# Kernel tuning notes

Measured on AMD Instinct MI355X. Metric: run time of the kernel, lower is better.

The kernel has to match this reference:

```python
import jax, jax.numpy as jnp
import numpy as np

N, E, IN, OUT = 50000, 800000, 128, 128
R = 5  # num_rels + 1 (last slice is the self-loop weight)


def setup_inputs() -> dict:
    key = jax.random.key(0)
    k = jax.random.split(key, 6)
    x = jax.random.normal(k[0], (N, IN), jnp.float32)
    src = jax.random.randint(k[1], (E,), 0, N)
    dst = jax.random.randint(k[2], (E,), 0, N)
    rel = jax.random.randint(k[3], (E,), 0, R - 1)  # edge rel_type in [0, num_rels)
    xavier = np.sqrt(2.0) * np.sqrt(6.0 / (IN + OUT))  # gain('relu') * xavier bound scale
    weight = jax.random.uniform(k[4], (R, IN, OUT), jnp.float32, -xavier, xavier)
    bias = jax.random.uniform(k[5], (R, OUT), jnp.float32, -xavier, xavier)
    return dict(x=x, weight=weight, bias=bias, src=src, dst=dst, rel=rel)


def reference(x, weight, bias, src, dst, rel):
    num_nodes = x.shape[0]
    num_edge_rels = weight.shape[0] - 1
    x_src = x[src]  # [E, IN] per-edge source gather
    # Per-edge message: x_src @ weight[rel] + bias[rel].
    # Grouped-GEMM style: one dense GEMM per relation, select by mask
    # (avoids materializing [E, IN, OUT] per-edge weights).
    msg = jnp.zeros((src.shape[0], weight.shape[2]), x.dtype)
    for r in range(num_edge_rels):
        hr = x_src @ weight[r] + bias[r]  # [E, OUT]
        msg = jnp.where((rel == r)[:, None], hr, msg)
    # Max-aggregation onto destination nodes; DGL fills 0 for nodes w/o in-edges.
    agg = jax.ops.segment_max(msg, dst, num_segments=num_nodes)  # [N, OUT]
    deg = jax.ops.segment_sum(jnp.ones_like(dst, jnp.float32), dst, num_segments=num_nodes)
    agg = jnp.where((deg > 0)[:, None], agg, jnp.zeros((), x.dtype))
    # Self-loop transform with last weight/bias slice.
    h = x @ weight[-1] + bias[-1] + agg
    return h
```

## Files before the change

### kernel.cpp

```cpp
#include <hip/hip_runtime.h>

#define NNODES 50000
#define NEDGES 800000
#define DIM    128
#define NRELS  4
#define NBLK2  25
#define DBLK   128
#define NDB    (5*DBLK)
#define NFB    3125
#define EPB    12500
#define NHC    64
#define RNG    25000

typedef __attribute__((ext_vector_type(8))) short bf16x8;
typedef __attribute__((ext_vector_type(8))) unsigned short u16x8;
typedef __attribute__((ext_vector_type(4))) float f32x4;

#define SSRC_OFF 0
#define CNT_OFF  3200000
#define BSUM_OFF 3404800
#define RANK_OFF 3405056
#define PCNT_OFF 5005056
#define WT_OFF   11405056
#define XBF_OFF  11568896
#define H_OFF    24368896

__device__ __forceinline__ unsigned short f2bf(float f) {
  unsigned u = __float_as_uint(f);
  return (unsigned short)((u + 0x7FFFu + ((u >> 16) & 1u)) >> 16);
}

__global__ void k_prep(const float* __restrict__ x, unsigned short* __restrict__ xbf,
                       const float* __restrict__ W, unsigned short* __restrict__ Wt) {
  int i = blockIdx.x * blockDim.x + threadIdx.x;
  if (i < NNODES * DIM / 8) {
    const float4* p = (const float4*)x + i * 2;
    float4 v0 = p[0], v1 = p[1];
    u16x8 o;
    o[0] = f2bf(v0.x); o[1] = f2bf(v0.y); o[2] = f2bf(v0.z); o[3] = f2bf(v0.w);
    o[4] = f2bf(v1.x); o[5] = f2bf(v1.y); o[6] = f2bf(v1.z); o[7] = f2bf(v1.w);
    *(u16x8*)(xbf + i * 8) = o;
  }
  if (i < 5 * DIM * DIM) {
    int r = i >> 14, rem = i & 16383, k = rem >> 7, c = rem & 127;
    Wt[(r << 14) + (c << 7) + k] = f2bf(W[i]);
  }
}

__global__ __launch_bounds__(1024) void k_hist(const int* __restrict__ dst,
                                               unsigned short* __restrict__ rank,
                                               unsigned short* __restrict__ pcnt) {
  __shared__ unsigned lh[RNG / 2];
  int c = blockIdx.x >> 1;
  int r0 = (blockIdx.x & 1) * RNG;
  for (int i = threadIdx.x; i < RNG / 2; i += 1024) lh[i] = 0u;
  __syncthreads();
  int e0 = c * EPB;
  for (int e = e0 + threadIdx.x; e < e0 + EPB; e += 1024) {
    int d = dst[e] - r0;
    if ((unsigned)d < (unsigned)RNG) {
      unsigned old = atomicAdd(&lh[d >> 1], (d & 1) ? 65536u : 1u);
      rank[e] = (unsigned short)((old >> ((d & 1) << 4)) & 0xFFFFu);
    }
  }
  __syncthreads();
  unsigned* prow = (unsigned*)(pcnt + (size_t)c * NNODES + r0);
  for (int i = threadIdx.x; i < RNG / 2; i += 1024) prow[i] = lh[i];
}

__global__ void k_scanB(unsigned short* __restrict__ pcnt, unsigned* __restrict__ cnt,
                        unsigned* __restrict__ bsum) {
  __shared__ unsigned sh[256];
  int tid = threadIdx.x;
  int bin0 = blockIdx.x * 2048 + tid * 8;
  unsigned run[8] = {0, 0, 0, 0, 0, 0, 0, 0};
  if (bin0 < NNODES) {
    for (int b = 0; b < NHC; b++) {
      size_t off = (size_t)b * NNODES + bin0;
      u16x8 v = *(const u16x8*)(pcnt + off);
      u16x8 w;
#pragma unroll
      for (int j = 0; j < 8; j++) { w[j] = (unsigned short)run[j]; run[j] += v[j]; }
      *(u16x8*)(pcnt + off) = w;
    }
  }
  unsigned tsum = 0;
#pragma unroll
  for (int j = 0; j < 8; j++) tsum += run[j];
  sh[tid] = tsum;
  __syncthreads();
  for (int off = 1; off < 256; off <<= 1) {
    unsigned t = (tid >= off) ? sh[tid - off] : 0u;
    __syncthreads();
    sh[tid] += t;
    __syncthreads();
  }
  unsigned r = sh[tid] - tsum;
#pragma unroll
  for (int j = 0; j < 8; j++) { unsigned t = run[j]; cnt[bin0 + j] = r; r += t; }
  if (tid == 255) bsum[blockIdx.x] = sh[255];
}

__global__ void k_fix(unsigned* __restrict__ cnt, const unsigned* __restrict__ bsum) {
  int blk = blockIdx.x;
  if (blk == 0) return;
  unsigned p = 0;
  for (int k = 0; k < blk; k++) p += bsum[k];
  int base = blk * 2048 + threadIdx.x * 8;
#pragma unroll
  for (int j = 0; j < 8; j++) cnt[base + j] += p;
}

__global__ __launch_bounds__(256, 2) void k_dfill(
    const unsigned short* __restrict__ xbf, const unsigned short* __restrict__ Wt,
    const float* __restrict__ bias, unsigned short* __restrict__ H,
    float* __restrict__ out, const int* __restrict__ rel, const int* __restrict__ dst,
    const int* __restrict__ src, const unsigned* __restrict__ cnt,
    const unsigned short* __restrict__ rank, const unsigned short* __restrict__ pfx,
    unsigned* __restrict__ ssrc) {
  if (blockIdx.x >= NDB) {
    int e = (blockIdx.x - NDB) * 256 + threadIdx.x;
    if (e < NEDGES) {
      int r = rel[e]; r = r < 0 ? 0 : (r > NRELS - 1 ? NRELS - 1 : r);
      int d = dst[e];
      unsigned pos = cnt[d] + (unsigned)pfx[(size_t)(e / EPB) * NNODES + d] + (unsigned)rank[e];
      ssrc[pos] = (unsigned)(r * NNODES + src[e]);
    }
    return;
  }
  __shared__ unsigned short st[4][2048];
  int lane = threadIdx.x & 63;
  int wv = threadIdx.x >> 6;
  int r = blockIdx.x / DBLK;
  const int NT = NNODES / 16;
  int col = lane & 15, quad = lane >> 4;

  const unsigned short* wr = Wt + (r << 14);
  bf16x8 B[8][4];
  float bs[8];
#pragma unroll
  for (int ct = 0; ct < 8; ct++) {
#pragma unroll
    for (int kk = 0; kk < 4; kk++)
      B[ct][kk] = *(const bf16x8*)(wr + ((ct * 16 + col) << 7) + kk * 32 + quad * 8);
    bs[ct] = bias[(r << 7) + ct * 16 + col];
  }

  for (int t = (blockIdx.x % DBLK) * 4 + wv; t < NT; t += DBLK * 4) {
    int n0 = t * 16;
    int na = n0 + col;
    bf16x8 a0 = *(const bf16x8*)(xbf + (na << 7) + quad * 8);
    bf16x8 a1 = *(const bf16x8*)(xbf + (na << 7) + 32 + quad * 8);
    bf16x8 a2 = *(const bf16x8*)(xbf + (na << 7) + 64 + quad * 8);
    bf16x8 a3 = *(const bf16x8*)(xbf + (na << 7) + 96 + quad * 8);

    if (r < NRELS) {
#pragma unroll
      for (int ct = 0; ct < 8; ct++) {
        f32x4 acc = {0.f, 0.f, 0.f, 0.f};
        acc = __builtin_amdgcn_mfma_f32_16x16x32_bf16(a0, B[ct][0], acc, 0, 0, 0);
        acc = __builtin_amdgcn_mfma_f32_16x16x32_bf16(a1, B[ct][1], acc, 0, 0, 0);
        acc = __builtin_amdgcn_mfma_f32_16x16x32_bf16(a2, B[ct][2], acc, 0, 0, 0);
        acc = __builtin_amdgcn_mfma_f32_16x16x32_bf16(a3, B[ct][3], acc, 0, 0, 0);
        int cc = ct * 16 + col;
#pragma unroll
        for (int j = 0; j < 4; j++) st[wv][(quad * 4 + j) * 128 + cc] = f2bf(acc[j] + bs[ct]);
      }
      unsigned short* gb = H + (((size_t)(r * NNODES + n0)) << 7);
#pragma unroll
      for (int s = 0; s < 4; s++) {
        int off = s * 512 + lane * 8;
        *(u16x8*)(gb + off) = *(const u16x8*)(&st[wv][off]);
      }
    } else {
#pragma unroll
      for (int ct = 0; ct < 8; ct++) {
        f32x4 acc = {0.f, 0.f, 0.f, 0.f};
        acc = __builtin_amdgcn_mfma_f32_16x16x32_bf16(a0, B[ct][0], acc, 0, 0, 0);
        acc = __builtin_amdgcn_mfma_f32_16x16x32_bf16(a1, B[ct][1], acc, 0, 0, 0);
        acc = __builtin_amdgcn_mfma_f32_16x16x32_bf16(a2, B[ct][2], acc, 0, 0, 0);
        acc = __builtin_amdgcn_mfma_f32_16x16x32_bf16(a3, B[ct][3], acc, 0, 0, 0);
        int cc = ct * 16 + col;
#pragma unroll
        for (int j = 0; j < 4; j++)
          out[((size_t)(n0 + quad * 4 + j) << 7) + (unsigned)cc] = acc[j] + bs[ct];
      }
    }
  }
}

__global__ __launch_bounds__(256, 4) void k_agg(
    const unsigned* __restrict__ cnt, const unsigned* __restrict__ ssrc,
    const uint2* __restrict__ H2, float* __restrict__ out) {
  int lane = threadIdx.x & 31;
  int half = threadIdx.x >> 5;
  int n = blockIdx.x * 8 + half;
  if (n >= NNODES) return;
  unsigned base = cnt[n];
  int deg = (int)(cnt[n + 1] - base);

  float m0 = -3.0e38f, m1 = -3.0e38f, m2 = -3.0e38f, m3 = -3.0e38f;
  int i = 0;
  for (; i + 4 <= deg; i += 4) {
    unsigned c0 = ssrc[base + i], c1 = ssrc[base + i + 1];
    unsigned c2 = ssrc[base + i + 2], c3 = ssrc[base + i + 3];
    uint2 v0 = H2[((size_t)c0 << 5) + lane];
    uint2 v1 = H2[((size_t)c1 << 5) + lane];
    uint2 v2 = H2[((size_t)c2 << 5) + lane];
    uint2 v3 = H2[((size_t)c3 << 5) + lane];
    m0 = fmaxf(m0, __uint_as_float(v0.x << 16));
    m1 = fmaxf(m1, __uint_as_float(v0.x & 0xFFFF0000u));
    m2 = fmaxf(m2, __uint_as_float(v0.y << 16));
    m3 = fmaxf(m3, __uint_as_float(v0.y & 0xFFFF0000u));
    m0 = fmaxf(m0, __uint_as_float(v1.x << 16));
    m1 = fmaxf(m1, __uint_as_float(v1.x & 0xFFFF0000u));
    m2 = fmaxf(m2, __uint_as_float(v1.y << 16));
    m3 = fmaxf(m3, __uint_as_float(v1.y & 0xFFFF0000u));
    m0 = fmaxf(m0, __uint_as_float(v2.x << 16));
    m1 = fmaxf(m1, __uint_as_float(v2.x & 0xFFFF0000u));
    m2 = fmaxf(m2, __uint_as_float(v2.y << 16));
    m3 = fmaxf(m3, __uint_as_float(v2.y & 0xFFFF0000u));
    m0 = fmaxf(m0, __uint_as_float(v3.x << 16));
    m1 = fmaxf(m1, __uint_as_float(v3.x & 0xFFFF0000u));
    m2 = fmaxf(m2, __uint_as_float(v3.y << 16));
    m3 = fmaxf(m3, __uint_as_float(v3.y & 0xFFFF0000u));
  }
  for (; i < deg; i++) {
    unsigned c = ssrc[base + i];
    uint2 v = H2[((size_t)c << 5) + lane];
    m0 = fmaxf(m0, __uint_as_float(v.x << 16));
    m1 = fmaxf(m1, __uint_as_float(v.x & 0xFFFF0000u));
    m2 = fmaxf(m2, __uint_as_float(v.y << 16));
    m3 = fmaxf(m3, __uint_as_float(v.y & 0xFFFF0000u));
  }
  float4* op = (float4*)(out + ((size_t)n << 7)) + lane;
  float4 s = *op;
  if (deg > 0) { s.x += m0; s.y += m1; s.z += m2; s.w += m3; }
  *op = s;
}

extern "C" void kernel_launch(void* const* d_in, const int* in_sizes, int n_in,
                              void* d_out, int out_size, void* d_ws, size_t ws_size,
                              hipStream_t stream) {
  const float* x = (const float*)d_in[0];
  const float* W = (const float*)d_in[1];
  const float* bias = (const float*)d_in[2];
  const int* src = (const int*)d_in[3];
  const int* dst = (const int*)d_in[4];
  const int* rel = (const int*)d_in[5];

  char* ws = (char*)d_ws;
  unsigned* ssrc = (unsigned*)(ws + SSRC_OFF);
  unsigned* cnt = (unsigned*)(ws + CNT_OFF);
  unsigned* bsum = (unsigned*)(ws + BSUM_OFF);
  unsigned short* rank = (unsigned short*)(ws + RANK_OFF);
  unsigned short* pcnt = (unsigned short*)(ws + PCNT_OFF);
  unsigned short* Wt = (unsigned short*)(ws + WT_OFF);
  unsigned short* xbf = (unsigned short*)(ws + XBF_OFF);
  unsigned short* H = (unsigned short*)(ws + H_OFF);
  float* out = (float*)d_out;

  hipLaunchKernelGGL(k_prep, dim3(3125), dim3(256), 0, stream, x, xbf, W, Wt);
  hipLaunchKernelGGL(k_hist, dim3(NHC * 2), dim3(1024), 0, stream, dst, rank, pcnt);
  hipLaunchKernelGGL(k_scanB, dim3(NBLK2), dim3(256), 0, stream, pcnt, cnt, bsum);
  hipLaunchKernelGGL(k_fix, dim3(NBLK2), dim3(256), 0, stream, cnt, bsum);
  hipLaunchKernelGGL(k_dfill, dim3(NDB + NFB), dim3(256), 0, stream, xbf, Wt, bias, H, out, rel,
                     dst, src, cnt, rank, pcnt, ssrc);
  hipLaunchKernelGGL(k_agg, dim3(6250), dim3(256), 0, stream, cnt, ssrc, (const uint2*)H, out);
}
```

Baseline: 188.9 us.

## Interleave GEMM and scatter blocks, widen aggregation loads to 16 bytes

The fused dense-GEMM / edge-scatter kernel now alternates GEMM and scatter blocks in the grid instead of running all GEMM blocks first. It also doubles the GEMM block count to 1280 (256 per relation). This is meant to overlap memory-bound scatter work with MFMA-bound GEMM work on each CU. The aggregation kernel now uses 16 lanes per node with uint4 loads, processing 16 nodes per block, to cut the number of load instructions per gathered row. In exchange, each lane holds more registers and fewer lanes are in flight per row.

```diff
diff --git a/kernel.cpp b/kernel.cpp
--- a/kernel.cpp
+++ b/kernel.cpp
@@ -5,8 +5,8 @@
 #define DIM    128
 #define NRELS  4
 #define NBLK2  25
-#define DBLK   128
-#define NDB    (5*DBLK)
+#define NDB    1280
+#define ILV    (2*NDB)
 #define NFB    3125
 #define EPB    12500
 #define NHC    64
@@ -118,8 +118,10 @@
     const int* __restrict__ src, const unsigned* __restrict__ cnt,
     const unsigned short* __restrict__ rank, const unsigned short* __restrict__ pfx,
     unsigned* __restrict__ ssrc) {
-  if (blockIdx.x >= NDB) {
-    int e = (blockIdx.x - NDB) * 256 + threadIdx.x;
+  int b = blockIdx.x;
+  if (b >= ILV || (b & 1)) {
+    int fi = (b < ILV) ? (b >> 1) : (b - NDB);
+    int e = fi * 256 + threadIdx.x;
     if (e < NEDGES) {
       int r = rel[e]; r = r < 0 ? 0 : (r > NRELS - 1 ? NRELS - 1 : r);
       int d = dst[e];
@@ -129,9 +131,11 @@
     return;
   }
   __shared__ unsigned short st[4][2048];
+  int di = b >> 1;
   int lane = threadIdx.x & 63;
   int wv = threadIdx.x >> 6;
-  int r = blockIdx.x / DBLK;
+  int r = di % 5;
+  int tl = di / 5;
   const int NT = NNODES / 16;
   int col = lane & 15, quad = lane >> 4;
 
@@ -146,7 +150,7 @@
     bs[ct] = bias[(r << 7) + ct * 16 + col];
   }
 
-  for (int t = (blockIdx.x % DBLK) * 4 + wv; t < NT; t += DBLK * 4) {
+  for (int t = tl * 4 + wv; t < NT; t += 1024) {
     int n0 = t * 16;
     int na = n0 + col;
     bf16x8 a0 = *(const bf16x8*)(xbf + (na << 7) + quad * 8);
@@ -191,52 +195,47 @@
 
 __global__ __launch_bounds__(256, 4) void k_agg(
     const unsigned* __restrict__ cnt, const unsigned* __restrict__ ssrc,
-    const uint2* __restrict__ H2, float* __restrict__ out) {
-  int lane = threadIdx.x & 31;
-  int half = threadIdx.x >> 5;
-  int n = blockIdx.x * 8 + half;
-  if (n >= NNODES) return;
+    const uint4* __restrict__ H4, float* __restrict__ out) {
+  int lane = threadIdx.x & 15;
+  int q = threadIdx.x >> 4;
+  int n = blockIdx.x * 16 + q;
   unsigned base = cnt[n];
   int deg = (int)(cnt[n + 1] - base);
 
   float m0 = -3.0e38f, m1 = -3.0e38f, m2 = -3.0e38f, m3 = -3.0e38f;
+  float m4 = -3.0e38f, m5 = -3.0e38f, m6 = -3.0e38f, m7 = -3.0e38f;
+#define UNP(v)                                        \
+  m0 = fmaxf(m0, __uint_as_float((v).x << 16));       \
+  m1 = fmaxf(m1, __uint_as_float((v).x & 0xFFFF0000u)); \
+  m2 = fmaxf(m2, __uint_as_float((v).y << 16));       \
+  m3 = fmaxf(m3, __uint_as_float((v).y & 0xFFFF0000u)); \
+  m4 = fmaxf(m4, __uint_as_float((v).z << 16));       \
+  m5 = fmaxf(m5, __uint_as_float((v).z & 0xFFFF0000u)); \
+  m6 = fmaxf(m6, __uint_as_float((v).w << 16));       \
+  m7 = fmaxf(m7, __uint_as_float((v).w & 0xFFFF0000u))
   int i = 0;
   for (; i + 4 <= deg; i += 4) {
     unsigned c0 = ssrc[base + i], c1 = ssrc[base + i + 1];
     unsigned c2 = ssrc[base + i + 2], c3 = ssrc[base + i + 3];
-    uint2 v0 = H2[((size_t)c0 << 5) + lane];
-    uint2 v1 = H2[((size_t)c1 << 5) + lane];
-    uint2 v2 = H2[((size_t)c2 << 5) + lane];
-    uint2 v3 = H2[((size_t)c3 << 5) + lane];
-    m0 = fmaxf(m0, __uint_as_float(v0.x << 16));
-    m1 = fmaxf(m1, __uint_as_float(v0.x & 0xFFFF0000u));
-    m2 = fmaxf(m2, __uint_as_float(v0.y << 16));
-    m3 = fmaxf(m3, __uint_as_float(v0.y & 0xFFFF0000u));
-    m0 = fmaxf(m0, __uint_as_float(v1.x << 16));
-    m1 = fmaxf(m1, __uint_as_float(v1.x & 0xFFFF0000u));
-    m2 = fmaxf(m2, __uint_as_float(v1.y << 16));
-    m3 = fmaxf(m3, __uint_as_float(v1.y & 0xFFFF0000u));
-    m0 = fmaxf(m0, __uint_as_float(v2.x << 16));
-    m1 = fmaxf(m1, __uint_as_float(v2.x & 0xFFFF0000u));
-    m2 = fmaxf(m2, __uint_as_float(v2.y << 16));
-    m3 = fmaxf(m3, __uint_as_float(v2.y & 0xFFFF0000u));
-    m0 = fmaxf(m0, __uint_as_float(v3.x << 16));
-    m1 = fmaxf(m1, __uint_as_float(v3.x & 0xFFFF0000u));
-    m2 = fmaxf(m2, __uint_as_float(v3.y << 16));
-    m3 = fmaxf(m3, __uint_as_float(v3.y & 0xFFFF0000u));
+    uint4 v0 = H4[((size_t)c0 << 4) + lane];
+    uint4 v1 = H4[((size_t)c1 << 4) + lane];
+    uint4 v2 = H4[((size_t)c2 << 4) + lane];
+    uint4 v3 = H4[((size_t)c3 << 4) + lane];
+    UNP(v0); UNP(v1); UNP(v2); UNP(v3);
   }
   for (; i < deg; i++) {
     unsigned c = ssrc[base + i];
-    uint2 v = H2[((size_t)c << 5) + lane];
-    m0 = fmaxf(m0, __uint_as_float(v.x << 16));
-    m1 = fmaxf(m1, __uint_as_float(v.x & 0xFFFF0000u));
-    m2 = fmaxf(m2, __uint_as_float(v.y << 16));
-    m3 = fmaxf(m3, __uint_as_float(v.y & 0xFFFF0000u));
-  }
-  float4* op = (float4*)(out + ((size_t)n << 7)) + lane;
-  float4 s = *op;
-  if (deg > 0) { s.x += m0; s.y += m1; s.z += m2; s.w += m3; }
-  *op = s;
+    uint4 v = H4[((size_t)c << 4) + lane];
+    UNP(v);
+  }
+#undef UNP
+  float4* op = (float4*)(out + ((size_t)n << 7)) + lane * 2;
+  float4 s0 = op[0], s1 = op[1];
+  if (deg > 0) {
+    s0.x += m0; s0.y += m1; s0.z += m2; s0.w += m3;
+    s1.x += m4; s1.y += m5; s1.z += m6; s1.w += m7;
+  }
+  op[0] = s0; op[1] = s1;
 }
 
 extern "C" void kernel_launch(void* const* d_in, const int* in_sizes, int n_in,
@@ -266,5 +265,5 @@
   hipLaunchKernelGGL(k_fix, dim3(NBLK2), dim3(256), 0, stream, cnt, bsum);
   hipLaunchKernelGGL(k_dfill, dim3(NDB + NFB), dim3(256), 0, stream, xbf, Wt, bias, H, out, rel,
                      dst, src, cnt, rank, pcnt, ssrc);
-  hipLaunchKernelGGL(k_agg, dim3(6250), dim3(256), 0, stream, cnt, ssrc, (const uint2*)H, out);
-}
+  hipLaunchKernelGGL(k_agg, dim3(3125), dim3(256), 0, stream, cnt, ssrc, (const uint4*)H, out);
+}
```

New measurement: 215.0 us. +13.8%, slower.
